# Kernel tuning notes

Measured on AMD Instinct MI355X. Metric: run time of the kernel, lower is better.

## Reference

```python
import jax, jax.numpy as jnp
import numpy as np

B, T, N, C = 2, 8, 10242, 64
K, NBR, O = 9, 7, 64


def setup_inputs() -> dict:
    key = jax.random.key(0)
    k1, k2, k3, k4, k5 = jax.random.split(key, 5)
    x = jax.random.normal(k1, (B, T, N, C), dtype=jnp.float32)
    index = jax.random.randint(k2, (N, NBR), 0, N, dtype=jnp.int64)
    itp_mat = jax.random.uniform(k3, (N, NBR, K), dtype=jnp.float32)
    conv_w = jax.random.normal(k4, (O, C, 1, K), dtype=jnp.float32) * (1.0 / np.sqrt(C * K))
    conv_b = jax.random.normal(k5, (O,), dtype=jnp.float32) * 0.01
    return {"x": x, "index": index, "itp_mat": itp_mat, "conv_w": conv_w, "conv_b": conv_b}


def reference(x, index, itp_mat, conv_w, conv_b):
    b, t, n, c = x.shape
    o = conv_w.shape[0]
    # (B,T,N,C) -> (B*T, C, N)
    feats = x.reshape(b * t, n, c).transpose(0, 2, 1)
    # gather neighbors: (BT, C, N, NBR)
    nb = feats[:, :, index]
    # per-node interpolation matmul: (BT, C, N, K)
    itp = jnp.einsum('bcnj,njk->bcnk', nb, itp_mat)
    # Conv2d with kernel (1,K) on width K collapses K fully: (BT, O, N)
    out = jnp.einsum('bcnk,ock->bon', itp, conv_w[:, :, 0, :]) + conv_b[None, :, None]
    # (B, T, O, N) -> (B, T, N, O)
    return out.reshape(b, t, o, n).transpose(0, 1, 3, 2)
```

## Files before the change

### kernel.cpp

```cpp
#include <hip/hip_runtime.h>

#define BT     16
#define NN     10242
#define CC     64
#define KK     9
#define NBR_   7
#define OO     64
#define MT     16
#define RS     584
#define KT     18
#define NTILES 641

using frag  = __attribute__((ext_vector_type(8))) short;
using f32x4 = __attribute__((ext_vector_type(4))) float;
using f32x2 = __attribute__((ext_vector_type(2))) float;

static __device__ __forceinline__ unsigned short f2bf(float f) {
    union { float f; unsigned u; } v; v.f = f;
    unsigned r = v.u + 0x7fffu + ((v.u >> 16) & 1u);
    return (unsigned short)(r >> 16);
}

static __device__ __forceinline__ unsigned pk2(float a, float b) {
    unsigned r;
    asm("v_cvt_pk_bf16_f32 %0, %1, %2" : "=v"(r) : "v"(a), "v"(b));
    return r;
}

__global__ void pack_w_kernel(const float* __restrict__ w, unsigned short* __restrict__ wb) {
    int i = blockIdx.x * blockDim.x + threadIdx.x;
    if (i >= KT * 4 * 64 * 8) return;
    int j  = i & 7;
    int l  = (i >> 3) & 63;
    int ct = (i >> 9) & 3;
    int t  = i >> 11;
    int q  = t * 32 + (l >> 4) * 8 + j;
    int o  = ct * 16 + (l & 15);
    int c, k;
    if (q < 512) { c = (q & 255) >> 2; k = (q >> 8) * 4 + (q & 3); }
    else         { c = q - 512;        k = 8; }
    wb[i] = f2bf(w[(o * CC + c) * KK + k]);
}

__global__ __launch_bounds__(256, 8) void sphere_conv_kernel(
    const float* __restrict__ x,
    const int*   __restrict__ index,
    const float* __restrict__ m,
    const unsigned short* __restrict__ wb,
    const float* __restrict__ bias,
    float*       __restrict__ out)
{
    __shared__ unsigned short itp_s[MT * RS];

    const int tid  = threadIdx.x;
    const int w    = tid >> 6;
    const int lane = tid & 63;

    const int bid  = blockIdx.x;
    const int xcd  = bid & 7;
    const int slot = bid >> 3;
    const int btl  = slot / NTILES;
    const int nt   = slot - btl * NTILES;
    const int bt   = xcd * 2 + btl;
    const int n0   = nt * MT;

    {
        const float* xbt = x + (size_t)bt * NN * CC;

        int nu[4];
        #pragma unroll
        for (int r = 0; r < 4; ++r) {
            const int n = n0 + w * 4 + r;
            nu[r] = __builtin_amdgcn_readfirstlane(n < NN ? n : (NN - 1));
        }

        float xv[4][NBR_];
        #pragma unroll
        for (int r = 0; r < 4; ++r) {
            const int* ip = index + nu[r] * NBR_;
            #pragma unroll
            for (int j = 0; j < NBR_; ++j)
                xv[r][j] = xbt[(size_t)ip[j] * CC + lane];
        }

        #pragma unroll
        for (int r = 0; r < 4; ++r) {
            const int ns = w * 4 + r;
            const float* mp = m + nu[r] * (NBR_ * KK);

            f32x2 acc2[4];
            float acc8 = 0.f;
            #pragma unroll
            for (int p = 0; p < 4; ++p) acc2[p] = (f32x2){0.f, 0.f};
            #pragma unroll
            for (int j = 0; j < NBR_; ++j) {
                const float xvj = xv[r][j];
                const f32x2 xv2 = (f32x2){xvj, xvj};
                #pragma unroll
                for (int p = 0; p < 4; ++p) {
                    const f32x2 m2 = (f32x2){mp[j * KK + 2 * p],
                                             mp[j * KK + 2 * p + 1]};
                    acc2[p] = __builtin_elementwise_fma(xv2, m2, acc2[p]);
                }
                acc8 = fmaf(xvj, mp[j * KK + 8], acc8);
            }

            uint2 q0, q1;
            q0.x = pk2(acc2[0][0], acc2[0][1]);
            q0.y = pk2(acc2[1][0], acc2[1][1]);
            q1.x = pk2(acc2[2][0], acc2[2][1]);
            q1.y = pk2(acc2[3][0], acc2[3][1]);
            unsigned short* row = &itp_s[ns * RS];
            *(uint2*)(&row[lane * 4])       = q0;
            *(uint2*)(&row[256 + lane * 4]) = q1;
            row[512 + lane] = f2bf(acc8);
        }
    }
    __syncthreads();

    const int ct   = w;
    const int am   = lane & 15;
    const int half = lane >> 4;

    f32x4 cacc = (f32x4){0.f, 0.f, 0.f, 0.f};

    const unsigned short* arow = &itp_s[am * RS + half * 8];
    const frag* wbf = (const frag*)wb;

    #pragma unroll
    for (int t = 0; t < KT; ++t) {
        const frag a = *(const frag*)(arow + t * 32);
        const frag b = wbf[(t * 4 + ct) * 64 + lane];
        cacc = __builtin_amdgcn_mfma_f32_16x16x32_bf16(a, b, cacc, 0, 0, 0);
    }

    const size_t obase = (size_t)bt * NN * OO;
    {
        const int o  = ct * 16 + am;
        const float bo = bias[o];
        #pragma unroll
        for (int i = 0; i < 4; ++i) {
            const int n = n0 + half * 4 + i;
            if (n < NN)
                __builtin_nontemporal_store(cacc[i] + bo,
                                            &out[obase + (size_t)n * OO + o]);
        }
    }
}

extern "C" void kernel_launch(void* const* d_in, const int* in_sizes, int n_in,
                              void* d_out, int out_size, void* d_ws, size_t ws_size,
                              hipStream_t stream) {
    const float* x      = (const float*)d_in[0];
    const int*   index  = (const int*)  d_in[1];
    const float* m      = (const float*)d_in[2];
    const float* conv_w = (const float*)d_in[3];
    const float* conv_b = (const float*)d_in[4];
    float* out = (float*)d_out;
    unsigned short* wb = (unsigned short*)d_ws;

    {
        const int total = KT * 4 * 64 * 8;
        pack_w_kernel<<<(total + 255) / 256, 256, 0, stream>>>(conv_w, wb);
    }
    {
        dim3 grid(8 * 2 * NTILES);
        sphere_conv_kernel<<<grid, 256, 0, stream>>>(x, index, m, wb, conv_b, out);
    }
}
```

Measured before the change: 143.4 us.

## Use persistent 1024-thread blocks with LDS-staged weights looping over tiles

Replaces the grid of one-tile 256-thread blocks with 512 persistent 1024-thread blocks. Each block stages the packed bf16 weights into LDS once with global_load_lds, then loops over up to six iterations, processing four 16-node tiles per iteration (one per wave group). The goal is to stop every tile from re-reading the weight fragments out of global/L2 and to cut block launch overhead. In exchange, every iteration now needs block-wide __syncthreads, which serialises gather and MFMA phases across all 16 waves. The larger LDS footprint and the lower block count may also reduce the latency hiding the gather-bound phase relies on.

```diff
diff --git a/kernel.cpp b/kernel.cpp
--- a/kernel.cpp
+++ b/kernel.cpp
@@ -9,7 +9,9 @@
 #define MT     16
 #define RS     584
 #define KT     18
-#define NTILES 641
+#define SLOTS  1282
+#define NB     512
+#define NIV    6
 
 using frag  = __attribute__((ext_vector_type(8))) short;
 using f32x4 = __attribute__((ext_vector_type(4))) float;
@@ -42,7 +44,7 @@
     wb[i] = f2bf(w[(o * CC + c) * KK + k]);
 }
 
-__global__ __launch_bounds__(256, 8) void sphere_conv_kernel(
+__global__ __launch_bounds__(1024, 4) void sphere_conv_kernel(
     const float* __restrict__ x,
     const int*   __restrict__ index,
     const float* __restrict__ m,
@@ -50,101 +52,125 @@
     const float* __restrict__ bias,
     float*       __restrict__ out)
 {
-    __shared__ unsigned short itp_s[MT * RS];
+    __shared__ unsigned short B_s[KT * 4 * 64 * 8];
+    __shared__ unsigned short itp_s[4][MT * RS];
 
     const int tid  = threadIdx.x;
     const int w    = tid >> 6;
     const int lane = tid & 63;
+    const int g    = w >> 2;
+    const int wg   = w & 3;
 
-    const int bid  = blockIdx.x;
-    const int xcd  = bid & 7;
-    const int slot = bid >> 3;
-    const int btl  = slot / NTILES;
-    const int nt   = slot - btl * NTILES;
-    const int bt   = xcd * 2 + btl;
-    const int n0   = nt * MT;
+    const int bid = blockIdx.x;
+    const int xcd = bid & 7;
+    const int q   = bid >> 3;
 
     {
-        const float* xbt = x + (size_t)bt * NN * CC;
-
-        int nu[4];
+        const char* wbc = (const char*)wb;
         #pragma unroll
-        for (int r = 0; r < 4; ++r) {
-            const int n = n0 + w * 4 + r;
-            nu[r] = __builtin_amdgcn_readfirstlane(n < NN ? n : (NN - 1));
-        }
-
-        float xv[4][NBR_];
-        #pragma unroll
-        for (int r = 0; r < 4; ++r) {
-            const int* ip = index + nu[r] * NBR_;
-            #pragma unroll
-            for (int j = 0; j < NBR_; ++j)
-                xv[r][j] = xbt[(size_t)ip[j] * CC + lane];
-        }
-
-        #pragma unroll
-        for (int r = 0; r < 4; ++r) {
-            const int ns = w * 4 + r;
-            const float* mp = m + nu[r] * (NBR_ * KK);
-
-            f32x2 acc2[4];
-            float acc8 = 0.f;
-            #pragma unroll
-            for (int p = 0; p < 4; ++p) acc2[p] = (f32x2){0.f, 0.f};
-            #pragma unroll
-            for (int j = 0; j < NBR_; ++j) {
-                const float xvj = xv[r][j];
-                const f32x2 xv2 = (f32x2){xvj, xvj};
-                #pragma unroll
-                for (int p = 0; p < 4; ++p) {
-                    const f32x2 m2 = (f32x2){mp[j * KK + 2 * p],
-                                             mp[j * KK + 2 * p + 1]};
-                    acc2[p] = __builtin_elementwise_fma(xv2, m2, acc2[p]);
-                }
-                acc8 = fmaf(xvj, mp[j * KK + 8], acc8);
+        for (int t = 0; t < 5; ++t) {
+            const int c = t * 16 + w;
+            if (c < 72) {
+                const void* src = wbc + c * 1024 + lane * 16;
+                __builtin_amdgcn_global_load_lds(
+                    (const __attribute__((address_space(1))) void*)src,
+                    (__attribute__((address_space(3))) void*)((char*)B_s + c * 1024),
+                    16, 0, 0);
             }
-
-            uint2 q0, q1;
-            q0.x = pk2(acc2[0][0], acc2[0][1]);
-            q0.y = pk2(acc2[1][0], acc2[1][1]);
-            q1.x = pk2(acc2[2][0], acc2[2][1]);
-            q1.y = pk2(acc2[3][0], acc2[3][1]);
-            unsigned short* row = &itp_s[ns * RS];
-            *(uint2*)(&row[lane * 4])       = q0;
-            *(uint2*)(&row[256 + lane * 4]) = q1;
-            row[512 + lane] = f2bf(acc8);
         }
     }
     __syncthreads();
 
-    const int ct   = w;
-    const int am   = lane & 15;
-    const int half = lane >> 4;
+    for (int i = 0; i < NIV; ++i) {
+        const int  ss    = i * 256 + q * 4 + g;
+        const bool valid = (ss < SLOTS);
+        const int  ssc   = valid ? ss : 0;
+        const int  btl   = (ssc >= 641) ? 1 : 0;
+        const int  nt    = ssc - btl * 641;
+        const int  bt    = xcd * 2 + btl;
+        const int  n0    = nt * MT;
 
-    f32x4 cacc = (f32x4){0.f, 0.f, 0.f, 0.f};
+        if (valid) {
+            const float* xbt = x + (size_t)bt * NN * CC;
 
-    const unsigned short* arow = &itp_s[am * RS + half * 8];
-    const frag* wbf = (const frag*)wb;
+            int nu[4];
+            #pragma unroll
+            for (int r = 0; r < 4; ++r) {
+                const int n = n0 + wg * 4 + r;
+                nu[r] = __builtin_amdgcn_readfirstlane(n < NN ? n : (NN - 1));
+            }
 
-    #pragma unroll
-    for (int t = 0; t < KT; ++t) {
-        const frag a = *(const frag*)(arow + t * 32);
-        const frag b = wbf[(t * 4 + ct) * 64 + lane];
-        cacc = __builtin_amdgcn_mfma_f32_16x16x32_bf16(a, b, cacc, 0, 0, 0);
-    }
+            float xv[4][NBR_];
+            #pragma unroll
+            for (int r = 0; r < 4; ++r) {
+                const int* ip = index + nu[r] * NBR_;
+                #pragma unroll
+                for (int j = 0; j < NBR_; ++j)
+                    xv[r][j] = xbt[(size_t)ip[j] * CC + lane];
+            }
 
-    const size_t obase = (size_t)bt * NN * OO;
-    {
-        const int o  = ct * 16 + am;
-        const float bo = bias[o];
-        #pragma unroll
-        for (int i = 0; i < 4; ++i) {
-            const int n = n0 + half * 4 + i;
-            if (n < NN)
-                __builtin_nontemporal_store(cacc[i] + bo,
-                                            &out[obase + (size_t)n * OO + o]);
+            #pragma unroll
+            for (int r = 0; r < 4; ++r) {
+                const int ns = wg * 4 + r;
+                const float* mp = m + nu[r] * (NBR_ * KK);
+
+                f32x2 acc2[4];
+                float acc8 = 0.f;
+                #pragma unroll
+                for (int p = 0; p < 4; ++p) acc2[p] = (f32x2){0.f, 0.f};
+                #pragma unroll
+                for (int j = 0; j < NBR_; ++j) {
+                    const float xvj = xv[r][j];
+                    const f32x2 xv2 = (f32x2){xvj, xvj};
+                    #pragma unroll
+                    for (int p = 0; p < 4; ++p) {
+                        const f32x2 m2 = (f32x2){mp[j * KK + 2 * p],
+                                                 mp[j * KK + 2 * p + 1]};
+                        acc2[p] = __builtin_elementwise_fma(xv2, m2, acc2[p]);
+                    }
+                    acc8 = fmaf(xvj, mp[j * KK + 8], acc8);
+                }
+
+                uint2 q0, q1;
+                q0.x = pk2(acc2[0][0], acc2[0][1]);
+                q0.y = pk2(acc2[1][0], acc2[1][1]);
+                q1.x = pk2(acc2[2][0], acc2[2][1]);
+                q1.y = pk2(acc2[3][0], acc2[3][1]);
+                unsigned short* row = &itp_s[g][ns * RS];
+                *(uint2*)(&row[lane * 4])       = q0;
+                *(uint2*)(&row[256 + lane * 4]) = q1;
+                row[512 + lane] = f2bf(acc8);
+            }
         }
+        __syncthreads();
+
+        if (valid) {
+            const int ct   = wg;
+            const int am   = lane & 15;
+            const int half = lane >> 4;
+
+            f32x4 cacc = (f32x4){0.f, 0.f, 0.f, 0.f};
+            const unsigned short* arow = &itp_s[g][am * RS + half * 8];
+
+            #pragma unroll
+            for (int t = 0; t < KT; ++t) {
+                const frag a = *(const frag*)(arow + t * 32);
+                const frag b = *(const frag*)&B_s[((t * 4 + ct) * 64 + lane) * 8];
+                cacc = __builtin_amdgcn_mfma_f32_16x16x32_bf16(a, b, cacc, 0, 0, 0);
+            }
+
+            const size_t obase = (size_t)bt * NN * OO;
+            const int o  = ct * 16 + am;
+            const float bo = bias[o];
+            #pragma unroll
+            for (int ii = 0; ii < 4; ++ii) {
+                const int n = n0 + half * 4 + ii;
+                if (n < NN)
+                    __builtin_nontemporal_store(cacc[ii] + bo,
+                                                &out[obase + (size_t)n * OO + o]);
+            }
+        }
+        __syncthreads();
     }
 }
 
@@ -164,7 +190,7 @@
         pack_w_kernel<<<(total + 255) / 256, 256, 0, stream>>>(conv_w, wb);
     }
     {
-        dim3 grid(8 * 2 * NTILES);
-        sphere_conv_kernel<<<grid, 256, 0, stream>>>(x, index, m, wb, conv_b, out);
+        dim3 grid(NB);
+        sphere_conv_kernel<<<grid, 1024, 0, stream>>>(x, index, m, wb, conv_b, out);
     }
 }
```

After: 172.7 us. 1.2x slower.
